# Performance work log

Measured on AMD Instinct MI355X. Metric: run time of the kernel, lower is better.

## Reference

```python
import jax, jax.numpy as jnp
import numpy as np

B, H, W, C, NH, K = 4, 56, 56, 128, 4, 7


def setup_inputs() -> dict:
    key = jax.random.key(0)
    ks = jax.random.split(key, 6)
    x = jax.random.normal(ks[0], (B, H, W, C), dtype=jnp.float32)
    w_qkv = jax.random.normal(ks[1], (C, 3 * C), dtype=jnp.float32) * 0.02
    b_qkv = jnp.zeros((3 * C,), dtype=jnp.float32)
    rpb = jax.random.normal(ks[2], (NH, 2 * K - 1, 2 * K - 1), dtype=jnp.float32) * 0.02
    w_proj = jax.random.normal(ks[3], (C, C), dtype=jnp.float32) * 0.02
    b_proj = jnp.zeros((C,), dtype=jnp.float32)
    return {"x": x, "w_qkv": w_qkv, "b_qkv": b_qkv, "rpb": rpb,
            "w_proj": w_proj, "b_proj": b_proj}


def reference(x, w_qkv, b_qkv, rpb, w_proj, b_proj):
    B_, H_, W_, C_ = x.shape
    nh = rpb.shape[0]
    k = (rpb.shape[1] + 1) // 2          # kernel_size
    hd = C_ // nh                        # head_dim
    nb = k // 2                          # neighborhood radius
    scale = hd ** -0.5

    qkv = (x @ w_qkv + b_qkv).reshape(B_, H_, W_, 3, nh, hd)
    q = qkv[:, :, :, 0].transpose(0, 3, 1, 2, 4) * scale   # [B,nh,H,W,hd]
    kk = qkv[:, :, :, 1].transpose(0, 3, 1, 2, 4)          # [B,nh,H,W,hd]
    v = qkv[:, :, :, 2].transpose(0, 3, 1, 2, 4)           # [B,nh,H,W,hd]

    # NATTEN window start indices: window clamped to stay in-bounds (query shifts off-center at edges)
    si = jnp.clip(jnp.arange(H_) - nb, 0, H_ - k)          # [H]
    sj = jnp.clip(jnp.arange(W_) - nb, 0, W_ - k)          # [W]
    idx_i = si[:, None] + jnp.arange(k)                    # [H,k] absolute key rows
    idx_j = sj[:, None] + jnp.arange(k)                    # [W,k] absolute key cols

    # gather neighborhood keys/values: [B,nh,H,k,W,k,hd] (axes: b n i p j q d)
    k_win = kk[:, :, idx_i][:, :, :, :, idx_j]
    v_win = v[:, :, idx_i][:, :, :, :, idx_j]

    # relative position bias: index = key_pos - query_pos + (k-1)
    rel_i = idx_i - jnp.arange(H_)[:, None] + (k - 1)      # [H,k]
    rel_j = idx_j - jnp.arange(W_)[:, None] + (k - 1)      # [W,k]
    bias = rpb[:, rel_i][:, :, :, rel_j]                   # [nh,H,k,W,k]
    bias = bias.transpose(0, 1, 3, 2, 4)                   # [nh,H,W,k,k]

    attn = jnp.einsum('bnijd,bnipjqd->bnijpq', q, k_win) + bias[None]
    attn = jax.nn.softmax(attn.reshape(B_, nh, H_, W_, k * k), axis=-1)
    attn = attn.reshape(B_, nh, H_, W_, k, k)

    out = jnp.einsum('bnijpq,bnipjqd->bnijd', attn, v_win)  # [B,nh,H,W,hd]
    out = out.transpose(0, 2, 3, 1, 4).reshape(B_, H_, W_, C_)
    return out @ w_proj + b_proj
```

## Files before the change

### kernel.cpp

```cpp
#include <hip/hip_runtime.h>

#define BATCH 4
#define HH 56
#define WW 56
#define CC 128
#define NHD 4
#define HD 32
#define KS 7
#define NB 3
#define HWSZ (HH * WW)
#define RPBW 13
#define QKV_N 384
#define QKV_ELE ((size_t)BATCH * NHD * HWSZ * HD)

__global__ __launch_bounds__(256) void qkv_gemm(
    const float* __restrict__ x, const float* __restrict__ w,
    const float* __restrict__ bias,
    float* __restrict__ qb, float* __restrict__ kb, float* __restrict__ vb)
{
    __shared__ float As[32][68];
    __shared__ float Bs[32][132];

    const int tid = threadIdx.x;
    const int tx  = tid & 15;
    const int ty  = tid >> 4;
    const int m0  = blockIdx.x * 64;
    const int n0  = blockIdx.y * 128;

    float acc[4][8];
    {
        const float4 ba = *(const float4*)(bias + n0 + 4 * tx);
        const float4 bb = *(const float4*)(bias + n0 + 64 + 4 * tx);
        #pragma unroll
        for (int i = 0; i < 4; ++i) {
            acc[i][0] = ba.x; acc[i][1] = ba.y; acc[i][2] = ba.z; acc[i][3] = ba.w;
            acc[i][4] = bb.x; acc[i][5] = bb.y; acc[i][6] = bb.z; acc[i][7] = bb.w;
        }
    }

    for (int kc = 0; kc < 128; kc += 32) {
        #pragma unroll
        for (int t = tid; t < 512; t += 256) {
            const int row = t >> 3;
            const int k4  = t & 7;
            const float4 xv = *(const float4*)(x + (size_t)(m0 + row) * CC + kc + 4 * k4);
            As[4 * k4 + 0][row] = xv.x;
            As[4 * k4 + 1][row] = xv.y;
            As[4 * k4 + 2][row] = xv.z;
            As[4 * k4 + 3][row] = xv.w;
        }
        #pragma unroll
        for (int t = tid; t < 1024; t += 256) {
            const int kr = t >> 5;
            const int n4 = t & 31;
            *(float4*)&Bs[kr][4 * n4] =
                *(const float4*)(w + (size_t)(kc + kr) * QKV_N + n0 + 4 * n4);
        }
        __syncthreads();
        #pragma unroll
        for (int kk = 0; kk < 32; ++kk) {
            const float4 a0 = *(const float4*)&As[kk][4 * ty];
            const float4 b0 = *(const float4*)&Bs[kk][4 * tx];
            const float4 b1 = *(const float4*)&Bs[kk][64 + 4 * tx];
            const float av[4] = {a0.x, a0.y, a0.z, a0.w};
            const float bv[8] = {b0.x, b0.y, b0.z, b0.w, b1.x, b1.y, b1.z, b1.w};
            #pragma unroll
            for (int i = 0; i < 4; ++i)
                #pragma unroll
                for (int j = 0; j < 8; ++j)
                    acc[i][j] += av[i] * bv[j];
        }
        __syncthreads();
    }

    const int t     = n0 >> 7;
    float* dst      = (t == 0) ? qb : (t == 1) ? kb : vb;
    const float scl = (t == 0) ? 0.17677669529663687f : 1.0f;
    const int c0 = 4 * tx;
    const int c1 = 64 + 4 * tx;
    const int h0 = c0 >> 5, d0 = c0 & 31;
    const int h1 = c1 >> 5, d1 = c1 & 31;
    const int b  = m0 / HWSZ;
    #pragma unroll
    for (int i = 0; i < 4; ++i) {
        const int m  = m0 + 4 * ty + i;
        const int ij = m - b * HWSZ;
        float* p0 = dst + ((size_t)(b * NHD + h0) * HWSZ + ij) * HD + d0;
        float* p1 = dst + ((size_t)(b * NHD + h1) * HWSZ + ij) * HD + d1;
        *(float4*)p0 = make_float4(acc[i][0] * scl, acc[i][1] * scl,
                                   acc[i][2] * scl, acc[i][3] * scl);
        *(float4*)p1 = make_float4(acc[i][4] * scl, acc[i][5] * scl,
                                   acc[i][6] * scl, acc[i][7] * scl);
    }
}

__global__ __launch_bounds__(256) void natten_attn(
    const float* __restrict__ qb, const float* __restrict__ kb,
    const float* __restrict__ vb, const float* __restrict__ rpb,
    float* __restrict__ ob)
{
    __shared__ float4 Ks[8][197];
    __shared__ float4 Vs[8][197];
    __shared__ float rpbs[RPBW * RPBW];

    const int tid = threadIdx.x;
    const int qid = tid >> 2;
    const int sub = tid & 3;
    const int qi_l = qid >> 3;
    const int qj_l = qid & 7;
    const int ti = blockIdx.x / 7;
    const int tj = blockIdx.x % 7;
    const int head = blockIdx.y;
    const int b    = blockIdx.z;
    const int qi = ti * 8 + qi_l;
    const int qj = tj * 8 + qj_l;
    const int R0 = min(max(ti * 8 - NB, 0), HH - 14);
    const int C0 = min(max(tj * 8 - NB, 0), WW - 14);

    const size_t base = (size_t)(b * NHD + head) * HWSZ;

    if (tid < RPBW * RPBW) rpbs[tid] = rpb[head * (RPBW * RPBW) + tid];

    for (int idx = tid; idx < 1568; idx += 256) {
        const int pos = idx >> 3;
        const int c   = idx & 7;
        const int ri  = pos / 14;
        const int rj  = pos - ri * 14;
        const size_t g = (base + (size_t)(R0 + ri) * WW + (C0 + rj)) * HD;
        Ks[c][pos] = ((const float4*)(kb + g))[c];
        Vs[c][pos] = ((const float4*)(vb + g))[c];
    }

    const int c0 = sub * 2;
    const float4* qp = (const float4*)(qb + (base + (size_t)qi * WW + qj) * HD) + c0;
    const float4 q0 = qp[0];
    const float4 q1 = qp[1];

    const int si  = min(max(qi - NB, 0), HH - KS);
    const int sj  = min(max(qj - NB, 0), WW - KS);
    const int ri0 = si - R0;
    const int rj0 = sj - C0;
    const int oi  = si - qi + (KS - 1);
    const int oj  = sj - qj + (KS - 1);

    __syncthreads();

    float s[49];
    #pragma unroll
    for (int pi = 0; pi < 7; ++pi) {
        const int rowoff = (ri0 + pi) * 14 + rj0;
        const int boff   = (oi + pi) * RPBW + oj;
        #pragma unroll
        for (int pj = 0; pj < 7; ++pj) {
            const int pos = rowoff + pj;
            const float4 k0 = Ks[c0][pos];
            const float4 k1 = Ks[c0 + 1][pos];
            float d = q0.x * k0.x + q0.y * k0.y + q0.z * k0.z + q0.w * k0.w
                    + q1.x * k1.x + q1.y * k1.y + q1.z * k1.z + q1.w * k1.w;
            d += __shfl_xor(d, 1, 64);
            d += __shfl_xor(d, 2, 64);
            s[pi * 7 + pj] = d + rpbs[boff + pj];
        }
    }

    float m = s[0];
    #pragma unroll
    for (int p = 1; p < 49; ++p) m = fmaxf(m, s[p]);
    float l = 0.f;
    #pragma unroll
    for (int p = 0; p < 49; ++p) { s[p] = __expf(s[p] - m); l += s[p]; }
    const float inv = 1.f / l;

    float4 o0 = make_float4(0.f, 0.f, 0.f, 0.f);
    float4 o1 = make_float4(0.f, 0.f, 0.f, 0.f);
    #pragma unroll
    for (int pi = 0; pi < 7; ++pi) {
        const int rowoff = (ri0 + pi) * 14 + rj0;
        #pragma unroll
        for (int pj = 0; pj < 7; ++pj) {
            const int pos = rowoff + pj;
            const float wt = s[pi * 7 + pj];
            const float4 v0 = Vs[c0][pos];
            const float4 v1 = Vs[c0 + 1][pos];
            o0.x += wt * v0.x; o0.y += wt * v0.y; o0.z += wt * v0.z; o0.w += wt * v0.w;
            o1.x += wt * v1.x; o1.y += wt * v1.y; o1.z += wt * v1.z; o1.w += wt * v1.w;
        }
    }

    float* op = ob + ((size_t)b * HWSZ + (size_t)qi * WW + qj) * CC + head * HD + sub * 8;
    ((float4*)op)[0] = make_float4(o0.x * inv, o0.y * inv, o0.z * inv, o0.w * inv);
    ((float4*)op)[1] = make_float4(o1.x * inv, o1.y * inv, o1.z * inv, o1.w * inv);
}

__global__ __launch_bounds__(256) void proj_gemm(
    const float* __restrict__ a, const float* __restrict__ w,
    const float* __restrict__ bias, float* __restrict__ out)
{
    __shared__ float As[32][36];
    __shared__ float Bs[32][132];

    const int tid = threadIdx.x;
    const int tx  = tid & 15;
    const int ty  = tid >> 4;
    const int m0  = blockIdx.x * 32;

    float acc[2][8];
    {
        const float4 ba = *(const float4*)(bias + 4 * tx);
        const float4 bb = *(const float4*)(bias + 64 + 4 * tx);
        #pragma unroll
        for (int i = 0; i < 2; ++i) {
            acc[i][0] = ba.x; acc[i][1] = ba.y; acc[i][2] = ba.z; acc[i][3] = ba.w;
            acc[i][4] = bb.x; acc[i][5] = bb.y; acc[i][6] = bb.z; acc[i][7] = bb.w;
        }
    }

    for (int kc = 0; kc < 128; kc += 32) {
        {
            const int row = tid >> 3;
            const int k4  = tid & 7;
            const float4 xv = *(const float4*)(a + (size_t)(m0 + row) * CC + kc + 4 * k4);
            As[4 * k4 + 0][row] = xv.x;
            As[4 * k4 + 1][row] = xv.y;
            As[4 * k4 + 2][row] = xv.z;
            As[4 * k4 + 3][row] = xv.w;
        }
        #pragma unroll
        for (int t = tid; t < 1024; t += 256) {
            const int kr = t >> 5;
            const int n4 = t & 31;
            *(float4*)&Bs[kr][4 * n4] =
                *(const float4*)(w + (size_t)(kc + kr) * CC + 4 * n4);
        }
        __syncthreads();
        #pragma unroll
        for (int kk = 0; kk < 32; ++kk) {
            const float2 a0 = *(const float2*)&As[kk][2 * ty];
            const float4 b0 = *(const float4*)&Bs[kk][4 * tx];
            const float4 b1 = *(const float4*)&Bs[kk][64 + 4 * tx];
            const float av[2] = {a0.x, a0.y};
            const float bv[8] = {b0.x, b0.y, b0.z, b0.w, b1.x, b1.y, b1.z, b1.w};
            #pragma unroll
            for (int i = 0; i < 2; ++i)
                #pragma unroll
                for (int j = 0; j < 8; ++j)
                    acc[i][j] += av[i] * bv[j];
        }
        __syncthreads();
    }

    #pragma unroll
    for (int i = 0; i < 2; ++i) {
        const int m = m0 + 2 * ty + i;
        float* p = out + (size_t)m * CC;
        *(float4*)(p + 4 * tx)      = make_float4(acc[i][0], acc[i][1], acc[i][2], acc[i][3]);
        *(float4*)(p + 64 + 4 * tx) = make_float4(acc[i][4], acc[i][5], acc[i][6], acc[i][7]);
    }
}

extern "C" void kernel_launch(void* const* d_in, const int* in_sizes, int n_in,
                              void* d_out, int out_size, void* d_ws, size_t ws_size,
                              hipStream_t stream) {
    const float* x      = (const float*)d_in[0];
    const float* w_qkv  = (const float*)d_in[1];
    const float* b_qkv  = (const float*)d_in[2];
    const float* rpb    = (const float*)d_in[3];
    const float* w_proj = (const float*)d_in[4];
    const float* b_proj = (const float*)d_in[5];
    float* out = (float*)d_out;

    float* ws  = (float*)d_ws;
    float* qbf = ws;
    float* kbf = ws + QKV_ELE;
    float* vbf = ws + 2 * QKV_ELE;
    float* obf = ws + 3 * QKV_ELE;

    qkv_gemm<<<dim3(196, 3), 256, 0, stream>>>(x, w_qkv, b_qkv, qbf, kbf, vbf);
    natten_attn<<<dim3(49, NHD, BATCH), 256, 0, stream>>>(qbf, kbf, vbf, rpb, obf);
    proj_gemm<<<392, 256, 0, stream>>>(obf, w_proj, b_proj, out);
}
```

Baseline: 128.1 us.

## Move QKV and projection GEMMs to split-bf16 MFMA with pre-transposed weights

Replaces the FP32 scalar-FMA GEMMs for the QKV and output projections with MFMA bf16 kernels. Each operand is split into high and low bf16 parts and three MFMAs per tile approximate fp32 accuracy. A new prep kernel transposes and splits the weights every call, adding a launch. The main cost targeted is ALU-bound fp32 FMA throughput in the GEMMs. Scalar (non-vector) output stores and the extra launch could offset some of the gain, while attention remains unchanged.

Result: faster. 110.9 us (-13.4%).

```diff
diff --git a/kernel.cpp b/kernel.cpp
--- a/kernel.cpp
+++ b/kernel.cpp
@@ -13,84 +13,132 @@
 #define QKV_N 384
 #define QKV_ELE ((size_t)BATCH * NHD * HWSZ * HD)
 
-__global__ __launch_bounds__(256) void qkv_gemm(
-    const float* __restrict__ x, const float* __restrict__ w,
-    const float* __restrict__ bias,
+typedef unsigned short u16;
+typedef unsigned int   u32;
+typedef short bf16x8 __attribute__((ext_vector_type(8)));
+typedef float f32x4  __attribute__((ext_vector_type(4)));
+
+static __device__ __forceinline__ u32 f2bf(float f) {
+    u32 u = __float_as_uint(f);
+    return (u + 0x7FFFu + ((u >> 16) & 1u)) >> 16;
+}
+static __device__ __forceinline__ float bf2f(u32 h) { return __uint_as_float(h << 16); }
+
+__global__ __launch_bounds__(256) void prep_w(
+    const float* __restrict__ w_qkv, const float* __restrict__ w_proj,
+    u16* __restrict__ wqT_h, u16* __restrict__ wqT_l,
+    u16* __restrict__ wpT_h, u16* __restrict__ wpT_l)
+{
+    const int e = blockIdx.x * 256 + threadIdx.x;
+    float v; u16 *dh, *dl; int idx;
+    if (e < 384 * 128) {
+        const int n = e >> 7, k = e & 127;
+        v = w_qkv[k * QKV_N + n];
+        dh = wqT_h; dl = wqT_l; idx = e;
+    } else {
+        const int e2 = e - 384 * 128;
+        const int n = e2 >> 7, k = e2 & 127;
+        v = w_proj[k * CC + n];
+        dh = wpT_h; dl = wpT_l; idx = e2;
+    }
+    const u32 h = f2bf(v);
+    dh[idx] = (u16)h;
+    dl[idx] = (u16)f2bf(v - bf2f(h));
+}
+
+#define LP 72
+
+__global__ __launch_bounds__(256) void qkv_mfma(
+    const float* __restrict__ x, const u16* __restrict__ wT_h,
+    const u16* __restrict__ wT_l, const float* __restrict__ bias,
     float* __restrict__ qb, float* __restrict__ kb, float* __restrict__ vb)
 {
-    __shared__ float As[32][68];
-    __shared__ float Bs[32][132];
-
-    const int tid = threadIdx.x;
-    const int tx  = tid & 15;
-    const int ty  = tid >> 4;
-    const int m0  = blockIdx.x * 64;
-    const int n0  = blockIdx.y * 128;
-
-    float acc[4][8];
-    {
-        const float4 ba = *(const float4*)(bias + n0 + 4 * tx);
-        const float4 bb = *(const float4*)(bias + n0 + 64 + 4 * tx);
-        #pragma unroll
-        for (int i = 0; i < 4; ++i) {
-            acc[i][0] = ba.x; acc[i][1] = ba.y; acc[i][2] = ba.z; acc[i][3] = ba.w;
-            acc[i][4] = bb.x; acc[i][5] = bb.y; acc[i][6] = bb.z; acc[i][7] = bb.w;
-        }
-    }
-
-    for (int kc = 0; kc < 128; kc += 32) {
-        #pragma unroll
-        for (int t = tid; t < 512; t += 256) {
-            const int row = t >> 3;
-            const int k4  = t & 7;
-            const float4 xv = *(const float4*)(x + (size_t)(m0 + row) * CC + kc + 4 * k4);
-            As[4 * k4 + 0][row] = xv.x;
-            As[4 * k4 + 1][row] = xv.y;
-            As[4 * k4 + 2][row] = xv.z;
-            As[4 * k4 + 3][row] = xv.w;
-        }
-        #pragma unroll
-        for (int t = tid; t < 1024; t += 256) {
-            const int kr = t >> 5;
-            const int n4 = t & 31;
-            *(float4*)&Bs[kr][4 * n4] =
-                *(const float4*)(w + (size_t)(kc + kr) * QKV_N + n0 + 4 * n4);
+    __shared__ __align__(16) u16 Ah[64 * LP], Al[64 * LP];
+    __shared__ __align__(16) u16 Bh[128 * LP], Bl[128 * LP];
+
+    const int tid  = threadIdx.x;
+    const int lane = tid & 63;
+    const int w    = tid >> 6;
+    const int wr = w >> 1, wc = w & 1;
+    const int lr = lane >> 4, lc = lane & 15;
+    const int m0 = blockIdx.x * 64;
+    const int tz = blockIdx.y;
+
+    f32x4 acc[2][4];
+    #pragma unroll
+    for (int nt = 0; nt < 4; ++nt) {
+        const float bn = bias[tz * 128 + wc * 64 + nt * 16 + lc];
+        acc[0][nt] = (f32x4){bn, bn, bn, bn};
+        acc[1][nt] = acc[0][nt];
+    }
+
+    for (int kc = 0; kc < 128; kc += 64) {
+        #pragma unroll
+        for (int it = 0; it < 4; ++it) {
+            const int task = tid + it * 256;
+            const int row = task >> 4, q4 = task & 15;
+            const float4 xv = *(const float4*)(x + (size_t)(m0 + row) * CC + kc + 4 * q4);
+            const u32 h0 = f2bf(xv.x), h1 = f2bf(xv.y), h2 = f2bf(xv.z), h3 = f2bf(xv.w);
+            const u32 l0 = f2bf(xv.x - bf2f(h0)), l1 = f2bf(xv.y - bf2f(h1));
+            const u32 l2 = f2bf(xv.z - bf2f(h2)), l3 = f2bf(xv.w - bf2f(h3));
+            const int off = row * LP + 4 * q4;
+            *(uint2*)&Ah[off] = make_uint2(h0 | (h1 << 16), h2 | (h3 << 16));
+            *(uint2*)&Al[off] = make_uint2(l0 | (l1 << 16), l2 | (l3 << 16));
+        }
+        #pragma unroll
+        for (int it = 0; it < 8; ++it) {
+            const int task = tid + it * 256;
+            const int hl = task >> 10;
+            const int t2 = task & 1023;
+            const int n = t2 >> 3, q8 = t2 & 7;
+            const u16* src = (hl ? wT_l : wT_h) + (size_t)(tz * 128 + n) * CC + kc + 8 * q8;
+            const uint4 vv = *(const uint4*)src;
+            u16* dst = (hl ? Bl : Bh) + n * LP + 8 * q8;
+            *(uint4*)dst = vv;
         }
         __syncthreads();
         #pragma unroll
-        for (int kk = 0; kk < 32; ++kk) {
-            const float4 a0 = *(const float4*)&As[kk][4 * ty];
-            const float4 b0 = *(const float4*)&Bs[kk][4 * tx];
-            const float4 b1 = *(const float4*)&Bs[kk][64 + 4 * tx];
-            const float av[4] = {a0.x, a0.y, a0.z, a0.w};
-            const float bv[8] = {b0.x, b0.y, b0.z, b0.w, b1.x, b1.y, b1.z, b1.w};
+        for (int s = 0; s < 2; ++s) {
+            const int ko = 32 * s + 8 * lr;
+            bf16x8 bfh[4], bfl[4];
             #pragma unroll
-            for (int i = 0; i < 4; ++i)
+            for (int nt = 0; nt < 4; ++nt) {
+                const int bo = (wc * 64 + nt * 16 + lc) * LP + ko;
+                bfh[nt] = *(const bf16x8*)&Bh[bo];
+                bfl[nt] = *(const bf16x8*)&Bl[bo];
+            }
+            #pragma unroll
+            for (int mt = 0; mt < 2; ++mt) {
+                const int ao = (wr * 32 + mt * 16 + lc) * LP + ko;
+                const bf16x8 afh = *(const bf16x8*)&Ah[ao];
+                const bf16x8 afl = *(const bf16x8*)&Al[ao];
                 #pragma unroll
-                for (int j = 0; j < 8; ++j)
-                    acc[i][j] += av[i] * bv[j];
+                for (int nt = 0; nt < 4; ++nt) {
+                    acc[mt][nt] = __builtin_amdgcn_mfma_f32_16x16x32_bf16(afh, bfh[nt], acc[mt][nt], 0, 0, 0);
+                    acc[mt][nt] = __builtin_amdgcn_mfma_f32_16x16x32_bf16(afh, bfl[nt], acc[mt][nt], 0, 0, 0);
+                    acc[mt][nt] = __builtin_amdgcn_mfma_f32_16x16x32_bf16(afl, bfh[nt], acc[mt][nt], 0, 0, 0);
+                }
+            }
         }
         __syncthreads();
     }
 
-    const int t     = n0 >> 7;
-    float* dst      = (t == 0) ? qb : (t == 1) ? kb : vb;
-    const float scl = (t == 0) ? 0.17677669529663687f : 1.0f;
-    const int c0 = 4 * tx;
-    const int c1 = 64 + 4 * tx;
-    const int h0 = c0 >> 5, d0 = c0 & 31;
-    const int h1 = c1 >> 5, d1 = c1 & 31;
-    const int b  = m0 / HWSZ;
-    #pragma unroll
-    for (int i = 0; i < 4; ++i) {
-        const int m  = m0 + 4 * ty + i;
-        const int ij = m - b * HWSZ;
-        float* p0 = dst + ((size_t)(b * NHD + h0) * HWSZ + ij) * HD + d0;
-        float* p1 = dst + ((size_t)(b * NHD + h1) * HWSZ + ij) * HD + d1;
-        *(float4*)p0 = make_float4(acc[i][0] * scl, acc[i][1] * scl,
-                                   acc[i][2] * scl, acc[i][3] * scl);
-        *(float4*)p1 = make_float4(acc[i][4] * scl, acc[i][5] * scl,
-                                   acc[i][6] * scl, acc[i][7] * scl);
+    float* dst      = (tz == 0) ? qb : (tz == 1) ? kb : vb;
+    const float scl = (tz == 0) ? 0.17677669529663687f : 1.0f;
+    const int b = m0 / HWSZ;
+    #pragma unroll
+    for (int mt = 0; mt < 2; ++mt) {
+        #pragma unroll
+        for (int nt = 0; nt < 4; ++nt) {
+            const int n = wc * 64 + nt * 16 + lc;
+            const int head = n >> 5, d = n & 31;
+            #pragma unroll
+            for (int r = 0; r < 4; ++r) {
+                const int m  = m0 + wr * 32 + mt * 16 + lr * 4 + r;
+                const int ij = m - b * HWSZ;
+                dst[((size_t)(b * NHD + head) * HWSZ + ij) * HD + d] = acc[mt][nt][r] * scl;
+            }
+        }
     }
 }
 
@@ -192,69 +240,80 @@
     ((float4*)op)[1] = make_float4(o1.x * inv, o1.y * inv, o1.z * inv, o1.w * inv);
 }
 
-__global__ __launch_bounds__(256) void proj_gemm(
-    const float* __restrict__ a, const float* __restrict__ w,
-    const float* __restrict__ bias, float* __restrict__ out)
+__global__ __launch_bounds__(256) void proj_mfma(
+    const float* __restrict__ a, const u16* __restrict__ wT_h,
+    const u16* __restrict__ wT_l, const float* __restrict__ bias,
+    float* __restrict__ out)
 {
-    __shared__ float As[32][36];
-    __shared__ float Bs[32][132];
-
-    const int tid = threadIdx.x;
-    const int tx  = tid & 15;
-    const int ty  = tid >> 4;
-    const int m0  = blockIdx.x * 32;
-
-    float acc[2][8];
-    {
-        const float4 ba = *(const float4*)(bias + 4 * tx);
-        const float4 bb = *(const float4*)(bias + 64 + 4 * tx);
-        #pragma unroll
-        for (int i = 0; i < 2; ++i) {
-            acc[i][0] = ba.x; acc[i][1] = ba.y; acc[i][2] = ba.z; acc[i][3] = ba.w;
-            acc[i][4] = bb.x; acc[i][5] = bb.y; acc[i][6] = bb.z; acc[i][7] = bb.w;
-        }
-    }
-
-    for (int kc = 0; kc < 128; kc += 32) {
-        {
-            const int row = tid >> 3;
-            const int k4  = tid & 7;
-            const float4 xv = *(const float4*)(a + (size_t)(m0 + row) * CC + kc + 4 * k4);
-            As[4 * k4 + 0][row] = xv.x;
-            As[4 * k4 + 1][row] = xv.y;
-            As[4 * k4 + 2][row] = xv.z;
-            As[4 * k4 + 3][row] = xv.w;
-        }
-        #pragma unroll
-        for (int t = tid; t < 1024; t += 256) {
-            const int kr = t >> 5;
-            const int n4 = t & 31;
-            *(float4*)&Bs[kr][4 * n4] =
-                *(const float4*)(w + (size_t)(kc + kr) * CC + 4 * n4);
+    __shared__ __align__(16) u16 Ah[32 * LP], Al[32 * LP];
+    __shared__ __align__(16) u16 Bh[128 * LP], Bl[128 * LP];
+
+    const int tid  = threadIdx.x;
+    const int lane = tid & 63;
+    const int w    = tid >> 6;
+    const int wr = w >> 1, wc = w & 1;
+    const int lr = lane >> 4, lc = lane & 15;
+    const int m0 = blockIdx.x * 32;
+
+    f32x4 acc[4];
+    #pragma unroll
+    for (int nt = 0; nt < 4; ++nt) {
+        const float bn = bias[wc * 64 + nt * 16 + lc];
+        acc[nt] = (f32x4){bn, bn, bn, bn};
+    }
+
+    for (int kc = 0; kc < 128; kc += 64) {
+        #pragma unroll
+        for (int it = 0; it < 2; ++it) {
+            const int task = tid + it * 256;
+            const int row = task >> 4, q4 = task & 15;
+            const float4 xv = *(const float4*)(a + (size_t)(m0 + row) * CC + kc + 4 * q4);
+            const u32 h0 = f2bf(xv.x), h1 = f2bf(xv.y), h2 = f2bf(xv.z), h3 = f2bf(xv.w);
+            const u32 l0 = f2bf(xv.x - bf2f(h0)), l1 = f2bf(xv.y - bf2f(h1));
+            const u32 l2 = f2bf(xv.z - bf2f(h2)), l3 = f2bf(xv.w - bf2f(h3));
+            const int off = row * LP + 4 * q4;
+            *(uint2*)&Ah[off] = make_uint2(h0 | (h1 << 16), h2 | (h3 << 16));
+            *(uint2*)&Al[off] = make_uint2(l0 | (l1 << 16), l2 | (l3 << 16));
+        }
+        #pragma unroll
+        for (int it = 0; it < 8; ++it) {
+            const int task = tid + it * 256;
+            const int hl = task >> 10;
+            const int t2 = task & 1023;
+            const int n = t2 >> 3, q8 = t2 & 7;
+            const u16* src = (hl ? wT_l : wT_h) + (size_t)n * CC + kc + 8 * q8;
+            const uint4 vv = *(const uint4*)src;
+            u16* dst = (hl ? Bl : Bh) + n * LP + 8 * q8;
+            *(uint4*)dst = vv;
         }
         __syncthreads();
         #pragma unroll
-        for (int kk = 0; kk < 32; ++kk) {
-            const float2 a0 = *(const float2*)&As[kk][2 * ty];
-            const float4 b0 = *(const float4*)&Bs[kk][4 * tx];
-            const float4 b1 = *(const float4*)&Bs[kk][64 + 4 * tx];
-            const float av[2] = {a0.x, a0.y};
-            const float bv[8] = {b0.x, b0.y, b0.z, b0.w, b1.x, b1.y, b1.z, b1.w};
+        for (int s = 0; s < 2; ++s) {
+            const int ko = 32 * s + 8 * lr;
+            const int ao = (wr * 16 + lc) * LP + ko;
+            const bf16x8 afh = *(const bf16x8*)&Ah[ao];
+            const bf16x8 afl = *(const bf16x8*)&Al[ao];
             #pragma unroll
-            for (int i = 0; i < 2; ++i)
-                #pragma unroll
-                for (int j = 0; j < 8; ++j)
-                    acc[i][j] += av[i] * bv[j];
+            for (int nt = 0; nt < 4; ++nt) {
+                const int bo = (wc * 64 + nt * 16 + lc) * LP + ko;
+                const bf16x8 bh = *(const bf16x8*)&Bh[bo];
+                const bf16x8 bl = *(const bf16x8*)&Bl[bo];
+                acc[nt] = __builtin_amdgcn_mfma_f32_16x16x32_bf16(afh, bh, acc[nt], 0, 0, 0);
+                acc[nt] = __builtin_amdgcn_mfma_f32_16x16x32_bf16(afh, bl, acc[nt], 0, 0, 0);
+                acc[nt] = __builtin_amdgcn_mfma_f32_16x16x32_bf16(afl, bh, acc[nt], 0, 0, 0);
+            }
         }
         __syncthreads();
     }
 
     #pragma unroll
-    for (int i = 0; i < 2; ++i) {
-        const int m = m0 + 2 * ty + i;
-        float* p = out + (size_t)m * CC;
-        *(float4*)(p + 4 * tx)      = make_float4(acc[i][0], acc[i][1], acc[i][2], acc[i][3]);
-        *(float4*)(p + 64 + 4 * tx) = make_float4(acc[i][4], acc[i][5], acc[i][6], acc[i][7]);
+    for (int nt = 0; nt < 4; ++nt) {
+        const int n = wc * 64 + nt * 16 + lc;
+        #pragma unroll
+        for (int r = 0; r < 4; ++r) {
+            const int m = m0 + wr * 16 + lr * 4 + r;
+            out[(size_t)m * CC + n] = acc[nt][r];
+        }
     }
 }
 
@@ -274,8 +333,13 @@
     float* kbf = ws + QKV_ELE;
     float* vbf = ws + 2 * QKV_ELE;
     float* obf = ws + 3 * QKV_ELE;
-
-    qkv_gemm<<<dim3(196, 3), 256, 0, stream>>>(x, w_qkv, b_qkv, qbf, kbf, vbf);
+    u16* wqT_h = (u16*)(ws + 4 * QKV_ELE);
+    u16* wqT_l = wqT_h + 384 * 128;
+    u16* wpT_h = wqT_l + 384 * 128;
+    u16* wpT_l = wpT_h + 128 * 128;
+
+    prep_w<<<256, 256, 0, stream>>>(w_qkv, w_proj, wqT_h, wqT_l, wpT_h, wpT_l);
+    qkv_mfma<<<dim3(196, 3), 256, 0, stream>>>(x, wqT_h, wqT_l, b_qkv, qbf, kbf, vbf);
     natten_attn<<<dim3(49, NHD, BATCH), 256, 0, stream>>>(qbf, kbf, vbf, rpb, obf);
-    proj_gemm<<<392, 256, 0, stream>>>(obf, w_proj, b_proj, out);
-}
+    proj_mfma<<<392, 256, 0, stream>>>(obf, wpT_h, wpT_l, b_proj, out);
+}
```
